# Kernel optimization log

Measured on AMD Instinct MI355X. Metric: run time of the kernel, lower is better.

The kernel has to match this reference:

```python
import jax, jax.numpy as jnp
import numpy as np
from math import log

X_SIZE, Y_SIZE, W_SIZE = 512, 512, 256
SIGMA = 2.0
TIME_CONST = 1000.0 / log(SIGMA)  # default time_constant = 1000/log(sigma)


def setup_inputs() -> dict:
    key = jax.random.key(0)
    k1, k2 = jax.random.split(key)
    x = jax.random.normal(k1, (W_SIZE,), dtype=jnp.float32)
    W = jax.random.normal(k2, (X_SIZE, Y_SIZE, W_SIZE), dtype=jnp.float32)
    return {"x": x, "W": W, "time_step": 100}


def reference(x, W, time_step):
    # per-cell L2 distance: (X_SIZE, Y_SIZE)
    d = jnp.linalg.norm(x - W, ord=2, axis=-1)
    flat = jnp.argmin(d)
    wx, wy = jnp.unravel_index(flat, (X_SIZE, Y_SIZE))
    # torch.meshgrid default 'ij' indexing
    GX, GY = jnp.meshgrid(
        jnp.arange(X_SIZE, dtype=jnp.float32),
        jnp.arange(Y_SIZE, dtype=jnp.float32),
        indexing="ij",
    )
    decay = SIGMA * jnp.exp(-jnp.float32(time_step) / TIME_CONST)
    denom = 2.0 * decay * decay
    # Faithful to torch: GX.T[wx, wy] == wy and GY.T[wx, wy] == wx
    distx = (GX - wy.astype(jnp.float32)) ** 2
    disty = (GY - wx.astype(jnp.float32)) ** 2
    h = (jnp.exp(-distx / denom) * jnp.exp(-disty / denom)).T
    return h, (wx, wy)
```

## Files before the change

kernel.cpp:

```cpp
#include <hip/hip_runtime.h>
#include <math.h>

#define XS 512
#define YS 512
#define WDIM 256
#define NCELLS (XS * YS)
#define K1_BLOCKS 2048
#define K1_THREADS 256
#define NSLOTS 32
#define SLOT_STRIDE 16

typedef float vfloat4 __attribute__((ext_vector_type(4)));

__global__ __launch_bounds__(K1_THREADS) void som_dist_kernel(
    const float* __restrict__ x,
    const float* __restrict__ W,
    unsigned long long* __restrict__ ws) {
  const int lane = threadIdx.x & 63;
  const int waveInBlock = threadIdx.x >> 6;
  const int gw = blockIdx.x * (K1_THREADS / 64) + waveInBlock;

  const vfloat4 xv = ((const vfloat4*)x)[lane];

  float bestD = 3.4e38f;
  int bestI = 0;

  const int base = gw * 32;
  const int r3 = lane & 3;

#pragma unroll 2
  for (int b = 0; b < 8; ++b) {
    const int cb = base + b * 4;
    const vfloat4* row = (const vfloat4*)(W + (size_t)cb * WDIM) + lane;
    const vfloat4 w0 = row[0 * (WDIM / 4)];
    const vfloat4 w1 = row[1 * (WDIM / 4)];
    const vfloat4 w2 = row[2 * (WDIM / 4)];
    const vfloat4 w3 = row[3 * (WDIM / 4)];

    float d;
    float s0, s1, s2, s3;
    d = xv.x - w0.x; s0  = d * d;
    d = xv.y - w0.y; s0 += d * d;
    d = xv.z - w0.z; s0 += d * d;
    d = xv.w - w0.w; s0 += d * d;

    d = xv.x - w1.x; s1  = d * d;
    d = xv.y - w1.y; s1 += d * d;
    d = xv.z - w1.z; s1 += d * d;
    d = xv.w - w1.w; s1 += d * d;

    d = xv.x - w2.x; s2  = d * d;
    d = xv.y - w2.y; s2 += d * d;
    d = xv.z - w2.z; s2 += d * d;
    d = xv.w - w2.w; s2 += d * d;

    d = xv.x - w3.x; s3  = d * d;
    d = xv.y - w3.y; s3 += d * d;
    d = xv.z - w3.z; s3 += d * d;
    d = xv.w - w3.w; s3 += d * d;

    const bool b0 = (lane & 1) != 0;
    float keepA = b0 ? s1 : s0;
    float sendA = b0 ? s0 : s1;
    float t0 = keepA + __shfl_xor(sendA, 1, 64);
    float keepB = b0 ? s3 : s2;
    float sendB = b0 ? s2 : s3;
    float t1 = keepB + __shfl_xor(sendB, 1, 64);

    const bool b1 = (lane & 2) != 0;
    float keepC = b1 ? t1 : t0;
    float sendC = b1 ? t0 : t1;
    float v = keepC + __shfl_xor(sendC, 2, 64);

    v += __shfl_xor(v, 4, 64);
    v += __shfl_xor(v, 8, 64);
    v += __shfl_xor(v, 16, 64);
    v += __shfl_xor(v, 32, 64);

    if (v < bestD) { bestD = v; bestI = cb + r3; }
  }

  unsigned long long packed =
      ((unsigned long long)__float_as_uint(bestD) << 32) | (unsigned int)bestI;

#pragma unroll
  for (int off = 32; off > 0; off >>= 1) {
    const unsigned long long o = __shfl_xor(packed, off, 64);
    packed = (o < packed) ? o : packed;
  }

  __shared__ unsigned long long sbest[K1_THREADS / 64];
  if (lane == 0) sbest[waveInBlock] = packed;
  __syncthreads();
  if (threadIdx.x == 0) {
    unsigned long long m = sbest[0];
#pragma unroll
    for (int i = 1; i < K1_THREADS / 64; ++i) {
      const unsigned long long v2 = sbest[i];
      m = (v2 < m) ? v2 : m;
    }
    atomicMin(ws + (blockIdx.x & (NSLOTS - 1)) * SLOT_STRIDE, m);
  }
}

__global__ __launch_bounds__(256) void som_h_kernel(
    const unsigned long long* __restrict__ ws,
    const int* __restrict__ time_step,
    float* __restrict__ out) {
  const int t = threadIdx.x;
  const int lane = t & 63;

  unsigned long long v = ws[(lane & (NSLOTS - 1)) * SLOT_STRIDE];
#pragma unroll
  for (int off = 1; off < 32; off <<= 1) {
    const unsigned long long o = __shfl_xor(v, off, 64);
    v = (o < v) ? o : v;
  }

  const int flat = (int)(v & 0xFFFFFFFFULL);
  const int wx = flat >> 9;
  const int wy = flat & (YS - 1);

  const float ts = (float)(*time_step);
  const float TIME_CONST = 1442.6950408889634f;
  const float decay = 2.0f * expf(-ts / TIME_CONST);
  const float denom = 2.0f * decay * decay;
  const float inv = -1.0f / denom;

  const int e = blockIdx.x * 1024 + t * 4;
  const int i = e >> 9;
  const int j0 = e & (YS - 1);
  const float di = (float)(i - wx);
  const float di2 = di * di;

  const float d0 = (float)(j0 + 0 - wy);
  const float d1 = (float)(j0 + 1 - wy);
  const float d2 = (float)(j0 + 2 - wy);
  const float d3 = (float)(j0 + 3 - wy);
  vfloat4 r;
  r.x = expf((di2 + d0 * d0) * inv);
  r.y = expf((di2 + d1 * d1) * inv);
  r.z = expf((di2 + d2 * d2) * inv);
  r.w = expf((di2 + d3 * d3) * inv);
  ((vfloat4*)out)[e >> 2] = r;

  if (blockIdx.x == 0 && t == 0) {
    out[NCELLS] = (float)wx;
    out[NCELLS + 1] = (float)wy;
  }
}

extern "C" void kernel_launch(void* const* d_in, const int* in_sizes, int n_in,
                              void* d_out, int out_size, void* d_ws, size_t ws_size,
                              hipStream_t stream) {
  const float* x = (const float*)d_in[0];
  const float* W = (const float*)d_in[1];
  const int* ts = (const int*)d_in[2];
  float* out = (float*)d_out;
  unsigned long long* ws = (unsigned long long*)d_ws;

  (void)hipMemsetAsync(ws, 0xFF, NSLOTS * SLOT_STRIDE * 8, stream);
  som_dist_kernel<<<K1_BLOCKS, K1_THREADS, 0, stream>>>(x, W, ws);
  som_h_kernel<<<NCELLS / 1024, 256, 0, stream>>>(ws, ts, out);
}
```

Measured before the change: 362.6 us.

## Interleave wave rows across grid with register double-buffered nontemporal loads

Changes the distance kernel's access pattern so that each iteration reads a contiguous grid-wide stripe of rows, instead of each wave walking its own 32-row chunk. The loop is fully unrolled, and the next four rows are prefetched into a second register buffer while the current four are reduced. W is read with nontemporal loads to avoid polluting the cache. The aim is better DRAM streaming and more loads in flight, at the cost of extra registers, which may reduce occupancy.

```diff
diff --git a/kernel.cpp b/kernel.cpp
--- a/kernel.cpp
+++ b/kernel.cpp
@@ -7,6 +7,9 @@
 #define NCELLS (XS * YS)
 #define K1_BLOCKS 2048
 #define K1_THREADS 256
+#define NWAVES (K1_BLOCKS * (K1_THREADS / 64))
+#define CH 4
+#define NITERS (NCELLS / (NWAVES * CH))
 #define NSLOTS 32
 #define SLOT_STRIDE 16
 
@@ -25,41 +28,60 @@
   float bestD = 3.4e38f;
   int bestI = 0;
 
-  const int base = gw * 32;
   const int r3 = lane & 3;
+  const bool b0 = (lane & 1) != 0;
+  const bool b1 = (lane & 2) != 0;
 
-#pragma unroll 2
-  for (int b = 0; b < 8; ++b) {
-    const int cb = base + b * 4;
-    const vfloat4* row = (const vfloat4*)(W + (size_t)cb * WDIM) + lane;
-    const vfloat4 w0 = row[0 * (WDIM / 4)];
-    const vfloat4 w1 = row[1 * (WDIM / 4)];
-    const vfloat4 w2 = row[2 * (WDIM / 4)];
-    const vfloat4 w3 = row[3 * (WDIM / 4)];
+  vfloat4 buf[2][CH];
 
-    float d;
+  {
+    const vfloat4* p0 = (const vfloat4*)(W + (size_t)(gw * CH) * WDIM) + lane;
+#pragma unroll
+    for (int r = 0; r < CH; ++r)
+      buf[0][r] = __builtin_nontemporal_load(p0 + r * (WDIM / 4));
+  }
+
+#pragma unroll
+  for (int it = 0; it < NITERS; ++it) {
+    if (it < NITERS - 1) {
+      const vfloat4* pn =
+          (const vfloat4*)(W + ((size_t)(it + 1) * (NWAVES * CH) + (size_t)gw * CH) * WDIM) +
+          lane;
+#pragma unroll
+      for (int r = 0; r < CH; ++r)
+        buf[(it + 1) & 1][r] = __builtin_nontemporal_load(pn + r * (WDIM / 4));
+    }
+
+    const int cb = it * (NWAVES * CH) + gw * CH;
+
     float s0, s1, s2, s3;
-    d = xv.x - w0.x; s0  = d * d;
-    d = xv.y - w0.y; s0 += d * d;
-    d = xv.z - w0.z; s0 += d * d;
-    d = xv.w - w0.w; s0 += d * d;
+    {
+      const vfloat4 w0 = buf[it & 1][0];
+      const vfloat4 w1 = buf[it & 1][1];
+      const vfloat4 w2 = buf[it & 1][2];
+      const vfloat4 w3 = buf[it & 1][3];
+      float d;
+      d = xv.x - w0.x; s0  = d * d;
+      d = xv.y - w0.y; s0 += d * d;
+      d = xv.z - w0.z; s0 += d * d;
+      d = xv.w - w0.w; s0 += d * d;
 
-    d = xv.x - w1.x; s1  = d * d;
-    d = xv.y - w1.y; s1 += d * d;
-    d = xv.z - w1.z; s1 += d * d;
-    d = xv.w - w1.w; s1 += d * d;
+      d = xv.x - w1.x; s1  = d * d;
+      d = xv.y - w1.y; s1 += d * d;
+      d = xv.z - w1.z; s1 += d * d;
+      d = xv.w - w1.w; s1 += d * d;
 
-    d = xv.x - w2.x; s2  = d * d;
-    d = xv.y - w2.y; s2 += d * d;
-    d = xv.z - w2.z; s2 += d * d;
-    d = xv.w - w2.w; s2 += d * d;
+      d = xv.x - w2.x; s2  = d * d;
+      d = xv.y - w2.y; s2 += d * d;
+      d = xv.z - w2.z; s2 += d * d;
+      d = xv.w - w2.w; s2 += d * d;
 
-    d = xv.x - w3.x; s3  = d * d;
-    d = xv.y - w3.y; s3 += d * d;
-    d = xv.z - w3.z; s3 += d * d;
-    d = xv.w - w3.w; s3 += d * d;
+      d = xv.x - w3.x; s3  = d * d;
+      d = xv.y - w3.y; s3 += d * d;
+      d = xv.z - w3.z; s3 += d * d;
+      d = xv.w - w3.w; s3 += d * d;
+    }
 
-    const bool b0 = (lane & 1) != 0;
     float keepA = b0 ? s1 : s0;
     float sendA = b0 ? s0 : s1;
     float t0 = keepA + __shfl_xor(sendA, 1, 64);
@@ -67,7 +89,6 @@
     float sendB = b0 ? s2 : s3;
     float t1 = keepB + __shfl_xor(sendB, 1, 64);
 
-    const bool b1 = (lane & 2) != 0;
     float keepC = b1 ? t1 : t0;
     float sendC = b1 ? t0 : t1;
     float v = keepC + __shfl_xor(sendC, 2, 64);
```

Result: faster. 340.3 us (-6.1%).
